# Kernel optimization log

Measured on AMD Instinct MI355X. Metric: run time of the kernel, lower is better.

The kernel has to match this reference:

```python
import jax, jax.numpy as jnp
import numpy as np

RADIUS = 8
DIMS = (2, 3)


def box_filter_1d(x, dim, r):
    # cumsum along dim, then sliding-window sum via prefix-sum differences,
    # with zero padding at the edges (mirrors the torch cumsum+cat trick).
    cs = jnp.cumsum(x, axis=dim)
    cs = jnp.swapaxes(cs, dim, 0)
    head = cs[r:2 * r + 1]                       # left edge: partial windows
    mid = cs[2 * r + 1:] - cs[:-2 * r - 1]       # full windows
    tail = cs[-1:] - cs[-2 * r - 1:-r - 1]       # right edge: partial windows
    out = jnp.concatenate([head, mid, tail], axis=0)
    return jnp.swapaxes(out, dim, 0)


def setup_inputs() -> dict:
    key = jax.random.key(0)
    tensor = jax.random.normal(key, (8, 32, 512, 512), dtype=jnp.float32)
    return {"tensor": tensor}


def reference(tensor):
    out = tensor
    for dim in DIMS:  # fixed, small structural loop over filtered axes
        assert out.shape[dim] > 2 * RADIUS
        out = box_filter_1d(out, dim, RADIUS)
    return out
```

## Files before the change

kernel.cpp:

```cpp
#include <hip/hip_runtime.h>

#define RADIUS 8
#define N 512
#define TR 32
#define LSTRIDE (N + 1)

__global__ __launch_bounds__(512, 4)
void box_kernel(const float* __restrict__ in, float* __restrict__ out) {
    __shared__ float tile[TR * LSTRIDE];

    const int blk   = blockIdx.x;
    const int img   = blk >> 4;
    const int strip = blk & 15;
    const int r0    = strip * TR;
    const float* __restrict__ ibase = in  + (size_t)img * N * N;
    float* __restrict__       obase = out + (size_t)img * N * N;
    const int c = threadIdx.x;

    float x[TR + 2 * RADIUS];
#pragma unroll
    for (int k = 0; k < TR + 2 * RADIUS; ++k) {
        const int row = r0 + k - RADIUS;
        x[k] = (row >= 0 && row < N) ? ibase[(size_t)row * N + c] : 0.0f;
    }
    float vs = 0.0f;
#pragma unroll
    for (int k = 0; k <= 2 * RADIUS; ++k) vs += x[k];
#pragma unroll
    for (int i = 0; i < TR; ++i) {
        tile[i * LSTRIDE + c] = vs;
        if (i + 1 < TR) vs += x[i + 2 * RADIUS + 1] - x[i];
    }
    __syncthreads();

    const int hrow = threadIdx.x & (TR - 1);
    const int seg  = threadIdx.x >> 5;
    const int c0   = seg * 32;
    const float* trow = &tile[hrow * LSTRIDE];
    float h[32];
    float hs = 0.0f;
#pragma unroll
    for (int k = -RADIUS; k <= RADIUS; ++k) {
        const int col = c0 + k;
        if (col >= 0 && col < N) hs += trow[col];
    }
#pragma unroll
    for (int j = 0; j < 32; ++j) {
        h[j] = hs;
        const int ac = c0 + j + 1 + RADIUS;
        const int sc = c0 + j - RADIUS;
        const float a = (ac < N) ? trow[ac] : 0.0f;
        const float s = (sc >= 0) ? trow[sc] : 0.0f;
        hs += a - s;
    }
    __syncthreads();

    float* twrow = &tile[hrow * LSTRIDE];
#pragma unroll
    for (int j = 0; j < 32; ++j) twrow[c0 + j] = h[j];
    __syncthreads();

#pragma unroll
    for (int i = 0; i < TR; ++i) {
        obase[(size_t)(r0 + i) * N + c] = tile[i * LSTRIDE + c];
    }
}

extern "C" void kernel_launch(void* const* d_in, const int* in_sizes, int n_in,
                              void* d_out, int out_size, void* d_ws, size_t ws_size,
                              hipStream_t stream) {
    const float* in = (const float*)d_in[0];
    float* out = (float*)d_out;
    const int images = 8 * 32;
    dim3 grid(images * (N / TR));
    dim3 block(512);
    hipLaunchKernelGGL(box_kernel, grid, block, 0, stream, in, out);
}
```

Baseline: 108.6 us.

## Vectorize vertical pass with float2 loads and store horizontal results directly

The vertical pass now runs on half the threads, each loading float2 pairs of columns and keeping a 17-entry ring buffer for the running window sum. The horizontal pass writes float4 results straight to global memory, which removes the second LDS round trip and two barriers. The cost is that half the block sits idle during the vertical phase, and the float4 stores are strided across rows, so they may coalesce poorly. LDS stride changed to N+2 for float2 alignment.

Result: slower. 183.1 us (+68.6%).

```diff
diff --git a/kernel.cpp b/kernel.cpp
--- a/kernel.cpp
+++ b/kernel.cpp
@@ -3,7 +3,7 @@
 #define RADIUS 8
 #define N 512
 #define TR 32
-#define LSTRIDE (N + 1)
+#define LSTRIDE (N + 2)
 
 __global__ __launch_bounds__(512, 4)
 void box_kernel(const float* __restrict__ in, float* __restrict__ out) {
@@ -15,54 +15,54 @@
     const int r0    = strip * TR;
     const float* __restrict__ ibase = in  + (size_t)img * N * N;
     float* __restrict__       obase = out + (size_t)img * N * N;
-    const int c = threadIdx.x;
+    const int t = threadIdx.x;
 
-    float x[TR + 2 * RADIUS];
+    if (t < 256) {
+        const int c2 = t * 2;
+        float2 ring[17];
+        float sx = 0.0f, sy = 0.0f;
 #pragma unroll
-    for (int k = 0; k < TR + 2 * RADIUS; ++k) {
-        const int row = r0 + k - RADIUS;
-        x[k] = (row >= 0 && row < N) ? ibase[(size_t)row * N + c] : 0.0f;
-    }
-    float vs = 0.0f;
-#pragma unroll
-    for (int k = 0; k <= 2 * RADIUS; ++k) vs += x[k];
-#pragma unroll
-    for (int i = 0; i < TR; ++i) {
-        tile[i * LSTRIDE + c] = vs;
-        if (i + 1 < TR) vs += x[i + 2 * RADIUS + 1] - x[i];
+        for (int k = 0; k < TR + 2 * RADIUS; ++k) {
+            const int row = r0 + k - RADIUS;
+            float2 v = make_float2(0.0f, 0.0f);
+            if (row >= 0 && row < N)
+                v = *reinterpret_cast<const float2*>(ibase + (size_t)row * N + c2);
+            sx += v.x; sy += v.y;
+            if (k >= 17) { sx -= ring[k % 17].x; sy -= ring[k % 17].y; }
+            ring[k % 17] = v;
+            if (k >= 2 * RADIUS) {
+                const int i = k - 2 * RADIUS;
+                *reinterpret_cast<float2*>(&tile[i * LSTRIDE + c2]) =
+                    make_float2(sx, sy);
+            }
+        }
     }
     __syncthreads();
 
-    const int hrow = threadIdx.x & (TR - 1);
-    const int seg  = threadIdx.x >> 5;
+    const int hrow = t & (TR - 1);
+    const int seg  = t >> 5;
     const int c0   = seg * 32;
     const float* trow = &tile[hrow * LSTRIDE];
-    float h[32];
     float hs = 0.0f;
 #pragma unroll
     for (int k = -RADIUS; k <= RADIUS; ++k) {
         const int col = c0 + k;
         if (col >= 0 && col < N) hs += trow[col];
     }
+    float* orow = obase + (size_t)(r0 + hrow) * N;
+    float h[4];
 #pragma unroll
     for (int j = 0; j < 32; ++j) {
-        h[j] = hs;
+        h[j & 3] = hs;
         const int ac = c0 + j + 1 + RADIUS;
         const int sc = c0 + j - RADIUS;
-        const float a = (ac < N) ? trow[ac] : 0.0f;
-        const float s = (sc >= 0) ? trow[sc] : 0.0f;
-        hs += a - s;
-    }
-    __syncthreads();
-
-    float* twrow = &tile[hrow * LSTRIDE];
-#pragma unroll
-    for (int j = 0; j < 32; ++j) twrow[c0 + j] = h[j];
-    __syncthreads();
-
-#pragma unroll
-    for (int i = 0; i < TR; ++i) {
-        obase[(size_t)(r0 + i) * N + c] = tile[i * LSTRIDE + c];
+        const float a  = (ac < N) ? trow[ac] : 0.0f;
+        const float sb = (sc >= 0) ? trow[sc] : 0.0f;
+        hs += a - sb;
+        if ((j & 3) == 3) {
+            *reinterpret_cast<float4*>(orow + c0 + j - 3) =
+                make_float4(h[0], h[1], h[2], h[3]);
+        }
     }
 }
 
@@ -71,8 +71,7 @@
                               hipStream_t stream) {
     const float* in = (const float*)d_in[0];
     float* out = (float*)d_out;
-    const int images = 8 * 32;
-    dim3 grid(images * (N / TR));
+    dim3 grid(8 * 32 * (N / TR));
     dim3 block(512);
     hipLaunchKernelGGL(box_kernel, grid, block, 0, stream, in, out);
 }
```
